# Optimization experiments

Hardware: AMD Instinct MI355X
Metric: run time of the kernel (lower is better)

The kernel has to match this reference:

```python
import jax, jax.numpy as jnp
import numpy as np

V, C, L, H, FF, T_MAX = 50257, 768, 12, 12, 3072, 1024
D = C // H  # head_dim = 64
B, T = 4, 1024


def setup_inputs() -> dict:
    key = jax.random.key(0)
    ks = jax.random.split(key, 20)
    s = 0.02
    inp = {
        'input_ids': jax.random.randint(ks[0], (B, T), 0, V),
        'tok_emb': jax.random.normal(ks[1], (V, C), jnp.float32) * s,
        'pos_emb': jax.random.normal(ks[2], (T_MAX, C), jnp.float32) * s,
        # per-layer stacked params; linear weights stored [in, out] (torch W.T)
        'qkv_w': jax.random.normal(ks[3], (L, C, 3 * C), jnp.float32) * s,
        'qkv_b': jnp.zeros((L, 3 * C), jnp.float32),
        'proj_w': jax.random.normal(ks[4], (L, C, C), jnp.float32) * (s / np.sqrt(2 * L)),
        'proj_b': jnp.zeros((L, C), jnp.float32),
        'ln1_w': jnp.ones((L, C), jnp.float32),
        'ln1_b': jnp.zeros((L, C), jnp.float32),
        'ln2_w': jnp.ones((L, C), jnp.float32),
        'ln2_b': jnp.zeros((L, C), jnp.float32),
        'fc1_w': jax.random.normal(ks[5], (L, C, FF), jnp.float32) * s,
        'fc1_b': jnp.zeros((L, FF), jnp.float32),
        'fc2_w': jax.random.normal(ks[6], (L, FF, C), jnp.float32) * s,
        'fc2_b': jnp.zeros((L, C), jnp.float32),
        'lnf_w': jnp.ones((C,), jnp.float32),
        'lnf_b': jnp.zeros((C,), jnp.float32),
    }
    return inp


def _ln(x, w, b, eps=1e-5):
    mu = jnp.mean(x, axis=-1, keepdims=True)
    var = jnp.var(x, axis=-1, keepdims=True)
    return (x - mu) * jax.lax.rsqrt(var + eps) * w + b


def _gpt_forward(input_ids, tok_emb, pos_emb, qkv_w, qkv_b, proj_w, proj_b,
                 ln1_w, ln1_b, ln2_w, ln2_b, fc1_w, fc1_b, fc2_w, fc2_b,
                 lnf_w, lnf_b):
    Bc, Tc = input_ids.shape
    x = tok_emb[input_ids] + pos_emb[:Tc][None, :, :]  # [B,T,C]
    causal = jnp.tril(jnp.ones((Tc, Tc), bool))  # [T,T]
    scale = 1.0 / np.sqrt(D)

    def block(x, p):
        (qw, qb, pw, pb, l1w, l1b, l2w, l2b, f1w, f1b, f2w, f2b) = p
        h = _ln(x, l1w, l1b)
        qkv = h @ qw + qb  # [B,T,3C]
        q, k, v = jnp.split(qkv, 3, axis=-1)
        q = q.reshape(Bc, Tc, H, D)
        k = k.reshape(Bc, Tc, H, D)
        v = v.reshape(Bc, Tc, H, D)
        att = jnp.einsum('bqhd,bkhd->bhqk', q, k) * scale
        att = jnp.where(causal[None, None], att, -jnp.inf)
        att = jax.nn.softmax(att, axis=-1)
        o = jnp.einsum('bhqk,bkhd->bqhd', att, v).reshape(Bc, Tc, C)
        x = x + o @ pw + pb
        h2 = _ln(x, l2w, l2b)
        m = jax.nn.gelu(h2 @ f1w + f1b, approximate=False) @ f2w + f2b
        return x + m, None

    params = (qkv_w, qkv_b, proj_w, proj_b, ln1_w, ln1_b, ln2_w, ln2_b,
              fc1_w, fc1_b, fc2_w, fc2_b)
    x, _ = jax.lax.scan(block, x, params)
    x = _ln(x, lnf_w, lnf_b)
    logits = x @ tok_emb.T  # tied lm_head, no bias
    return logits


def reference(input_ids, tok_emb, pos_emb, qkv_w, qkv_b, proj_w, proj_b,
              ln1_w, ln1_b, ln2_w, ln2_b, fc1_w, fc1_b, fc2_w, fc2_b,
              lnf_w, lnf_b):
    return _gpt_forward(input_ids, tok_emb, pos_emb, qkv_w, qkv_b, proj_w,
                        proj_b, ln1_w, ln1_b, ln2_w, ln2_b, fc1_w, fc1_b,
                        fc2_w, fc2_b, lnf_w, lnf_b)
```

## Files before the change

kernel.cpp:

```cpp
#include <hip/hip_runtime.h>
#include <hip/hip_bf16.h>


typedef __bf16 bh_t;
typedef __bf16 bfx4 __attribute__((ext_vector_type(4)));
typedef __bf16 bfx8 __attribute__((ext_vector_type(8)));
typedef float  fx4  __attribute__((ext_vector_type(4)));

#define CDIM 768
#define TSEQ 1024
#define NHEAD 12
#define HDIM 64
#define NLAYER 12
#define MROWS 4096
#define VOCAB 50257
#define VPAD  50432

__device__ __forceinline__ void gload_lds16(const void* g, void* l) {
  __builtin_amdgcn_global_load_lds(
      (const __attribute__((address_space(1))) void*)g,
      (__attribute__((address_space(3))) void*)l, 16, 0, 0);
}

__device__ __forceinline__ fx4 mfma16(bfx8 a, bfx8 b, fx4 c) {
  return __builtin_amdgcn_mfma_f32_16x16x32_bf16(a, b, c, 0, 0, 0);
}

__global__ __launch_bounds__(512, 4) void gemm256n(
    const bh_t* __restrict__ A, const bh_t* __restrict__ B,
    const float* __restrict__ bias, void* __restrict__ outp,
    int M, int N, int K, int lda, int flags)
{
  __shared__ bh_t A0[256][32], B0s[128][32];
  __shared__ bh_t A1[256][32], B1s[128][32];
  const int tid = threadIdx.x;
  const int wid = tid >> 6, lane = tid & 63;
  const int g = lane >> 4, r16 = lane & 15;
  const int wr = wid >> 1, wc = wid & 1;
  const int m0 = blockIdx.x * 256, n0 = blockIdx.y * 128;
  const int swk = (g ^ ((r16 >> 1) & 3)) * 8;

  const bh_t* Ab = A + (size_t)blockIdx.z * K + (size_t)m0 * lda;
  const bh_t* Bb = B + (size_t)blockIdx.z * K + (size_t)n0 * lda;
  const int nt = K >> 5;

  fx4 acc[4][4] = {};

  auto stage = [&](bh_t* dA, bh_t* dB, int t) {
    const int k0 = t << 5;
    #pragma unroll
    for (int j = 0; j < 2; ++j) {
      const int idx = j * 512 + tid;
      const int row = idx >> 2;
      const int slot = (idx & 3) ^ ((row >> 1) & 3);
      gload_lds16(Ab + (size_t)row * lda + k0 + slot * 8, dA + (size_t)idx * 8);
    }
    {
      const int idx = tid;
      const int row = idx >> 2;
      const int slot = (idx & 3) ^ ((row >> 1) & 3);
      gload_lds16(Bb + (size_t)row * lda + k0 + slot * 8, dB + (size_t)idx * 8);
    }
  };

#define N_TILE(CA, CB, NA, NB, T)                                             \
  {                                                                           \
    if ((T) + 1 < nt) stage(&NA[0][0], &NB[0][0], (T) + 1);                   \
    bfx8 av[4], bv[4];                                                        \
    _Pragma("unroll")                                                         \
    for (int ni = 0; ni < 4; ++ni)                                            \
      bv[ni] = *(const bfx8*)(&CB[wc * 64 + ni * 16 + r16][0] + swk);         \
    _Pragma("unroll")                                                         \
    for (int mi = 0; mi < 4; ++mi)                                            \
      av[mi] = *(const bfx8*)(&CA[wr * 64 + mi * 16 + r16][0] + swk);         \
    asm volatile("s_waitcnt lgkmcnt(0)" ::: "memory");                        \
    __builtin_amdgcn_s_setprio(1);                                            \
    _Pragma("unroll")                                                         \
    for (int mi = 0; mi < 4; ++mi)                                            \
      _Pragma("unroll")                                                       \
      for (int ni = 0; ni < 4; ++ni)                                          \
        acc[mi][ni] = mfma16(av[mi], bv[ni], acc[mi][ni]);                    \
    __builtin_amdgcn_s_setprio(0);                                            \
    asm volatile("s_waitcnt vmcnt(0)" ::: "memory");                          \
    __builtin_amdgcn_s_barrier();                                             \
    asm volatile("" ::: "memory");                                            \
  }

  stage(&A0[0][0], &B0s[0][0], 0);
  asm volatile("s_waitcnt vmcnt(0)" ::: "memory");
  __builtin_amdgcn_s_barrier();
  asm volatile("" ::: "memory");

  for (int t = 0; t < nt; t += 2) {
    N_TILE(A0, B0s, A1, B1s, t);
    N_TILE(A1, B1s, A0, B0s, t + 1);
  }
#undef N_TILE

  const bool hasBias = flags & 1, doGelu = flags & 4, outBf = flags & 8;
  float* outF = (float*)outp + (size_t)blockIdx.z * ((size_t)M * N);
  bh_t*  outB = (bh_t*)outp;
  #pragma unroll
  for (int mi = 0; mi < 4; ++mi) {
    const int rowb = m0 + wr * 64 + mi * 16 + 4 * g;
    #pragma unroll
    for (int ni = 0; ni < 4; ++ni) {
      const int col = n0 + wc * 64 + ni * 16 + r16;
      if (col >= N) continue;
      const float bv = hasBias ? bias[col] : 0.0f;
      #pragma unroll
      for (int rr = 0; rr < 4; ++rr) {
        const size_t idx = (size_t)(rowb + rr) * N + col;
        float v = acc[mi][ni][rr] + bv;
        if (doGelu) v = 0.5f * v * (1.0f + erff(v * 0.70710678118654752f));
        if (outBf) outB[idx] = (bh_t)v; else outF[idx] = v;
      }
    }
  }
}

__global__ __launch_bounds__(256) void skred_ln(
    const float* __restrict__ part, const float* __restrict__ bias,
    float* __restrict__ x, const float* __restrict__ w,
    const float* __restrict__ bb, bh_t* __restrict__ out, int S)
{
  const int wave = threadIdx.x >> 6, lane = threadIdx.x & 63;
  const int row = blockIdx.x * 4 + wave;
  const size_t base = (size_t)row * CDIM;
  const int off = lane * 4;
  const size_t stride = (size_t)MROWS * CDIM;

  float4 v0 = *(const float4*)(x + base + off);
  float4 v1 = *(const float4*)(x + base + 256 + off);
  float4 v2 = *(const float4*)(x + base + 512 + off);
  for (int s = 0; s < S; ++s) {
    const float* pr = part + s * stride + base;
    const float4 p0 = *(const float4*)(pr + off);
    const float4 p1 = *(const float4*)(pr + 256 + off);
    const float4 p2 = *(const float4*)(pr + 512 + off);
    v0.x += p0.x; v0.y += p0.y; v0.z += p0.z; v0.w += p0.w;
    v1.x += p1.x; v1.y += p1.y; v1.z += p1.z; v1.w += p1.w;
    v2.x += p2.x; v2.y += p2.y; v2.z += p2.z; v2.w += p2.w;
  }
  const float4 q0 = *(const float4*)(bias + off);
  const float4 q1 = *(const float4*)(bias + 256 + off);
  const float4 q2 = *(const float4*)(bias + 512 + off);
  v0.x += q0.x; v0.y += q0.y; v0.z += q0.z; v0.w += q0.w;
  v1.x += q1.x; v1.y += q1.y; v1.z += q1.z; v1.w += q1.w;
  v2.x += q2.x; v2.y += q2.y; v2.z += q2.z; v2.w += q2.w;
  *(float4*)(x + base + off) = v0;
  *(float4*)(x + base + 256 + off) = v1;
  *(float4*)(x + base + 512 + off) = v2;

  float s1 = v0.x + v0.y + v0.z + v0.w + v1.x + v1.y + v1.z + v1.w
           + v2.x + v2.y + v2.z + v2.w;
  float ss = v0.x*v0.x + v0.y*v0.y + v0.z*v0.z + v0.w*v0.w
           + v1.x*v1.x + v1.y*v1.y + v1.z*v1.z + v1.w*v1.w
           + v2.x*v2.x + v2.y*v2.y + v2.z*v2.z + v2.w*v2.w;
  #pragma unroll
  for (int d = 1; d < 64; d <<= 1) { s1 += __shfl_xor(s1, d); ss += __shfl_xor(ss, d); }
  const float mean = s1 * (1.0f / 768.0f);
  const float inv = rsqrtf(ss * (1.0f / 768.0f) - mean * mean + 1e-5f);
  bh_t* orow = out + base;

  const float4 w0 = *(const float4*)(w + off),       b0 = *(const float4*)(bb + off);
  const float4 w1 = *(const float4*)(w + 256 + off), b1 = *(const float4*)(bb + 256 + off);
  const float4 w2 = *(const float4*)(w + 512 + off), b2 = *(const float4*)(bb + 512 + off);
  bfx4 o;
  o[0] = (bh_t)((v0.x - mean) * inv * w0.x + b0.x);
  o[1] = (bh_t)((v0.y - mean) * inv * w0.y + b0.y);
  o[2] = (bh_t)((v0.z - mean) * inv * w0.z + b0.z);
  o[3] = (bh_t)((v0.w - mean) * inv * w0.w + b0.w);
  *(bfx4*)(orow + off) = o;
  o[0] = (bh_t)((v1.x - mean) * inv * w1.x + b1.x);
  o[1] = (bh_t)((v1.y - mean) * inv * w1.y + b1.y);
  o[2] = (bh_t)((v1.z - mean) * inv * w1.z + b1.z);
  o[3] = (bh_t)((v1.w - mean) * inv * w1.w + b1.w);
  *(bfx4*)(orow + 256 + off) = o;
  o[0] = (bh_t)((v2.x - mean) * inv * w2.x + b2.x);
  o[1] = (bh_t)((v2.y - mean) * inv * w2.y + b2.y);
  o[2] = (bh_t)((v2.z - mean) * inv * w2.z + b2.z);
  o[3] = (bh_t)((v2.w - mean) * inv * w2.w + b2.w);
  *(bfx4*)(orow + 512 + off) = o;
}

__global__ __launch_bounds__(256) void attn_fwd(
    const bh_t* __restrict__ qkv, const bh_t* __restrict__ vT,
    bh_t* __restrict__ outb)
{
  __shared__ bh_t P[4][16][56];
  const int wave = threadIdx.x >> 6, lane = threadIdx.x & 63;
  const int g = lane >> 4, r16 = lane & 15;
  const int gw = blockIdx.x * 4 + wave;
  const int qblk = gw & 63;
  const int bh = gw >> 6;
  const int h = bh % NHEAD, b = bh / NHEAD;
  const int qbase = qblk * 16;
  const int qidx = qbase + r16;

  const bh_t* qp = qkv + (size_t)(b * TSEQ + qbase + r16) * (3 * CDIM) + h * HDIM + 8 * g;
  const bfx8 qf0 = *(const bfx8*)qp;
  const bfx8 qf1 = *(const bfx8*)(qp + 32);

  fx4 o[4] = {};
  float m = -INFINITY, l = 0.0f;
  const int ntiles = qblk / 2 + 1;

  for (int t = 0; t < ntiles; ++t) {
    const int kv0 = t * 32;
    const bh_t* kp = qkv + (size_t)(b * TSEQ + kv0 + r16) * (3 * CDIM) + CDIM + h * HDIM + 8 * g;
    const bfx8 ka0 = *(const bfx8*)kp;
    const bfx8 ka1 = *(const bfx8*)(kp + 32);
    const bfx8 kb0 = *(const bfx8*)(kp + 16 * (3 * CDIM));
    const bfx8 kb1 = *(const bfx8*)(kp + 16 * (3 * CDIM) + 32);
    fx4 s0 = {}, s1 = {};
    s0 = mfma16(ka0, qf0, s0); s0 = mfma16(ka1, qf1, s0);
    s1 = mfma16(kb0, qf0, s1); s1 = mfma16(kb1, qf1, s1);

    float mx = -INFINITY;
    float sv0[4], sv1[4];
    #pragma unroll
    for (int rr = 0; rr < 4; ++rr) {
      const int kva = kv0 + 4 * g + rr;
      const int kvb = kva + 16;
      sv0[rr] = (kva <= qidx) ? s0[rr] * 0.125f : -INFINITY;
      sv1[rr] = (kvb <= qidx) ? s1[rr] * 0.125f : -INFINITY;
      mx = fmaxf(mx, fmaxf(sv0[rr], sv1[rr]));
    }
    mx = fmaxf(mx, __shfl_xor(mx, 16));
    mx = fmaxf(mx, __shfl_xor(mx, 32));
    const float mnew = fmaxf(m, mx);
    const float corr = __expf(m - mnew);

    float ps = 0.0f;
    float pv0[4], pv1[4];
    #pragma unroll
    for (int rr = 0; rr < 4; ++rr) {
      pv0[rr] = __expf(sv0[rr] - mnew);
      pv1[rr] = __expf(sv1[rr] - mnew);
      ps += pv0[rr] + pv1[rr];
    }
    ps += __shfl_xor(ps, 16);
    ps += __shfl_xor(ps, 32);
    l = l * corr + ps;
    m = mnew;

    #pragma unroll
    for (int rr = 0; rr < 4; ++rr) {
      const float cr = __shfl(corr, 4 * g + rr);
      o[0][rr] *= cr; o[1][rr] *= cr; o[2][rr] *= cr; o[3][rr] *= cr;
    }

    bfx4 w0, w1;
    #pragma unroll
    for (int rr = 0; rr < 4; ++rr) { w0[rr] = (bh_t)pv0[rr]; w1[rr] = (bh_t)pv1[rr]; }
    *(bfx4*)&P[wave][r16][4 * g]      = w0;
    *(bfx4*)&P[wave][r16][16 + 4 * g] = w1;
    __builtin_amdgcn_wave_barrier();
    const bfx8 pf = *(const bfx8*)&P[wave][r16][8 * g];

    #pragma unroll
    for (int fi = 0; fi < 4; ++fi) {
      const bh_t* vp = vT + (size_t)(bh * HDIM + fi * 16 + r16) * TSEQ + kv0 + 8 * g;
      const bfx8 vf = *(const bfx8*)vp;
      o[fi] = mfma16(pf, vf, o[fi]);
    }
  }

  #pragma unroll
  for (int rr = 0; rr < 4; ++rr) {
    const float lr = __shfl(l, 4 * g + rr);
    const float inv = 1.0f / lr;
    const int trow = b * TSEQ + qbase + 4 * g + rr;
    #pragma unroll
    for (int fi = 0; fi < 4; ++fi)
      outb[(size_t)trow * CDIM + h * HDIM + fi * 16 + r16] = (bh_t)(o[fi][rr] * inv);
  }
}

__global__ __launch_bounds__(256) void ln_fwd(
    const float* __restrict__ x, const float* __restrict__ w,
    const float* __restrict__ bb, bh_t* __restrict__ out)
{
  const int wave = threadIdx.x >> 6, lane = threadIdx.x & 63;
  const int row = blockIdx.x * 4 + wave;
  const float* xr = x + (size_t)row * CDIM;
  const int off = lane * 4;
  const float4 v0 = *(const float4*)(xr + off);
  const float4 v1 = *(const float4*)(xr + 256 + off);
  const float4 v2 = *(const float4*)(xr + 512 + off);
  float s  = v0.x + v0.y + v0.z + v0.w + v1.x + v1.y + v1.z + v1.w
           + v2.x + v2.y + v2.z + v2.w;
  float ss = v0.x*v0.x + v0.y*v0.y + v0.z*v0.z + v0.w*v0.w
           + v1.x*v1.x + v1.y*v1.y + v1.z*v1.z + v1.w*v1.w
           + v2.x*v2.x + v2.y*v2.y + v2.z*v2.z + v2.w*v2.w;
  #pragma unroll
  for (int d = 1; d < 64; d <<= 1) { s += __shfl_xor(s, d); ss += __shfl_xor(ss, d); }
  const float mean = s * (1.0f / 768.0f);
  const float inv = rsqrtf(ss * (1.0f / 768.0f) - mean * mean + 1e-5f);
  bh_t* orow = out + (size_t)row * CDIM;

  const float4 w0 = *(const float4*)(w + off),  b0 = *(const float4*)(bb + off);
  const float4 w1 = *(const float4*)(w + 256 + off), b1 = *(const float4*)(bb + 256 + off);
  const float4 w2 = *(const float4*)(w + 512 + off), b2 = *(const float4*)(bb + 512 + off);
  bfx4 o;
  o[0] = (bh_t)((v0.x - mean) * inv * w0.x + b0.x);
  o[1] = (bh_t)((v0.y - mean) * inv * w0.y + b0.y);
  o[2] = (bh_t)((v0.z - mean) * inv * w0.z + b0.z);
  o[3] = (bh_t)((v0.w - mean) * inv * w0.w + b0.w);
  *(bfx4*)(orow + off) = o;
  o[0] = (bh_t)((v1.x - mean) * inv * w1.x + b1.x);
  o[1] = (bh_t)((v1.y - mean) * inv * w1.y + b1.y);
  o[2] = (bh_t)((v1.z - mean) * inv * w1.z + b1.z);
  o[3] = (bh_t)((v1.w - mean) * inv * w1.w + b1.w);
  *(bfx4*)(orow + 256 + off) = o;
  o[0] = (bh_t)((v2.x - mean) * inv * w2.x + b2.x);
  o[1] = (bh_t)((v2.y - mean) * inv * w2.y + b2.y);
  o[2] = (bh_t)((v2.z - mean) * inv * w2.z + b2.z);
  o[3] = (bh_t)((v2.w - mean) * inv * w2.w + b2.w);
  *(bfx4*)(orow + 512 + off) = o;
}

__global__ void embed_k(const int* __restrict__ ids, const float* __restrict__ tok,
                        const float* __restrict__ pos, float* __restrict__ x)
{
  const int bt = blockIdx.x;
  const int t = bt & (TSEQ - 1);
  const int id = ids[bt];
  const float* tr = tok + (size_t)id * CDIM;
  const float* pr = pos + (size_t)t * CDIM;
  float* xr = x + (size_t)bt * CDIM;
  for (int j = threadIdx.x; j < CDIM; j += 256) xr[j] = tr[j] + pr[j];
}

__global__ void tconv(const float* __restrict__ in, bh_t* __restrict__ out, int R, int Cn)
{
  __shared__ float tile[32][33];
  const size_t msz = (size_t)R * Cn;
  in  += msz * blockIdx.z;
  out += msz * blockIdx.z;
  const int tx = threadIdx.x & 31, ty = threadIdx.x >> 5;
  const int c0 = blockIdx.x * 32, r0 = blockIdx.y * 32;
  #pragma unroll
  for (int i = 0; i < 32; i += 8)
    tile[ty + i][tx] = in[(size_t)(r0 + ty + i) * Cn + c0 + tx];
  __syncthreads();
  #pragma unroll
  for (int i = 0; i < 32; i += 8)
    out[(size_t)(c0 + ty + i) * R + r0 + tx] = (bh_t)tile[tx][ty + i];
}

__global__ void embconv(const float* __restrict__ in, bh_t* __restrict__ out)
{
  const size_t i4 = ((size_t)blockIdx.x * 256 + threadIdx.x) * 4;
  if (i4 >= (size_t)VPAD * CDIM) return;
  const size_t vlim = (size_t)VOCAB * CDIM;
  float4 f = make_float4(0.f, 0.f, 0.f, 0.f);
  if (i4 < vlim) f = *(const float4*)(in + i4);
  bfx4 o;
  o[0] = (bh_t)f.x; o[1] = (bh_t)f.y; o[2] = (bh_t)f.z; o[3] = (bh_t)f.w;
  *(bfx4*)(out + i4) = o;
}

__global__ void vtrans(const bh_t* __restrict__ qkv, bh_t* __restrict__ vT)
{
  __shared__ bh_t tile[32][34];
  const int bh = blockIdx.z;
  const int b = bh / NHEAD, h = bh % NHEAD;
  const int d0 = blockIdx.x * 32, t0 = blockIdx.y * 32;
  const int tx = threadIdx.x & 31, ty = threadIdx.x >> 5;
  #pragma unroll
  for (int i = 0; i < 32; i += 8)
    tile[ty + i][tx] = qkv[(size_t)(b * TSEQ + t0 + ty + i) * (3 * CDIM) + 2 * CDIM + h * HDIM + d0 + tx];
  __syncthreads();
  #pragma unroll
  for (int i = 0; i < 32; i += 8)
    vT[(size_t)(bh * HDIM + d0 + ty + i) * TSEQ + t0 + tx] = tile[tx][ty + i];
}

extern "C" void kernel_launch(void* const* d_in, const int* in_sizes, int n_in,
                              void* d_out, int out_size, void* d_ws, size_t ws_size,
                              hipStream_t stream)
{
  (void)in_sizes; (void)n_in; (void)out_size; (void)ws_size;
  const int*   ids    = (const int*)d_in[0];
  const float* tok    = (const float*)d_in[1];
  const float* pos    = (const float*)d_in[2];
  const float* qkv_w  = (const float*)d_in[3];
  const float* qkv_b  = (const float*)d_in[4];
  const float* proj_w = (const float*)d_in[5];
  const float* proj_b = (const float*)d_in[6];
  const float* ln1_w  = (const float*)d_in[7];
  const float* ln1_b  = (const float*)d_in[8];
  const float* ln2_w  = (const float*)d_in[9];
  const float* ln2_b  = (const float*)d_in[10];
  const float* fc1_w  = (const float*)d_in[11];
  const float* fc1_b  = (const float*)d_in[12];
  const float* fc2_w  = (const float*)d_in[13];
  const float* fc2_b  = (const float*)d_in[14];
  const float* lnf_w  = (const float*)d_in[15];
  const float* lnf_b  = (const float*)d_in[16];

  char* wp = (char*)d_ws;
  auto carve = [&](size_t bytes) { char* p = wp; wp += (bytes + 255) & ~(size_t)255; return p; };
  float* x     = (float*)carve((size_t)MROWS * CDIM * 4);
  bh_t*  hbuf  = (bh_t*)carve((size_t)MROWS * CDIM * 2);
  bh_t*  qkvb  = (bh_t*)carve((size_t)MROWS * 3 * CDIM * 2);
  bh_t*  vT    = (bh_t*)carve((size_t)48 * HDIM * TSEQ * 2);
  bh_t*  attno = (bh_t*)carve((size_t)MROWS * CDIM * 2);
  bh_t*  mlp1  = (bh_t*)carve((size_t)MROWS * 3072 * 2);
  bh_t*  embT  = (bh_t*)carve((size_t)VPAD * CDIM * 2);

  char* op = (char*)d_out;
  auto carveO = [&](size_t bytes) { char* p = op; op += (bytes + 255) & ~(size_t)255; return p; };
  bh_t* qkvwT  = (bh_t*)carveO((size_t)NLAYER * 3 * CDIM * CDIM * 2);
  bh_t* projwT = (bh_t*)carveO((size_t)NLAYER * CDIM * CDIM * 2);
  bh_t* fc1wT  = (bh_t*)carveO((size_t)NLAYER * 3072 * CDIM * 2);
  bh_t* fc2wT  = (bh_t*)carveO((size_t)NLAYER * CDIM * 3072 * 2);
  float* skpart = (float*)carveO((size_t)4 * MROWS * CDIM * 4);

  tconv<<<dim3(2304 / 32, 768 / 32, NLAYER), 256, 0, stream>>>(qkv_w, qkvwT, 768, 2304);
  tconv<<<dim3(768 / 32, 768 / 32, NLAYER), 256, 0, stream>>>(proj_w, projwT, 768, 768);
  tconv<<<dim3(3072 / 32, 768 / 32, NLAYER), 256, 0, stream>>>(fc1_w, fc1wT, 768, 3072);
  tconv<<<dim3(768 / 32, 3072 / 32, NLAYER), 256, 0, stream>>>(fc2_w, fc2wT, 3072, 768);
  embconv<<<((VPAD * CDIM / 4) + 255) / 256, 256, 0, stream>>>(tok, embT);
  embed_k<<<MROWS, 256, 0, stream>>>(ids, tok, pos, x);

  ln_fwd<<<MROWS / 4, 256, 0, stream>>>(x, ln1_w, ln1_b, hbuf);
  for (int l = 0; l < NLAYER; ++l) {
    gemm256n<<<dim3(16, 18), 512, 0, stream>>>(hbuf, qkvwT + (size_t)l * 3 * CDIM * CDIM,
        qkv_b + l * 3 * CDIM, qkvb, MROWS, 3 * CDIM, CDIM, CDIM, 1 | 8);
    vtrans<<<dim3(2, 32, 48), 256, 0, stream>>>(qkvb, vT);
    attn_fwd<<<768, 256, 0, stream>>>(qkvb, vT, attno);
    gemm256n<<<dim3(16, 6, 4), 512, 0, stream>>>(attno,
        projwT + (size_t)l * CDIM * CDIM, nullptr, skpart, MROWS, CDIM, 192, CDIM, 0);
    skred_ln<<<MROWS / 4, 256, 0, stream>>>(skpart, proj_b + l * CDIM, x,
        ln2_w + l * CDIM, ln2_b + l * CDIM, hbuf, 4);
    gemm256n<<<dim3(16, 24), 512, 0, stream>>>(hbuf, fc1wT + (size_t)l * 3072 * CDIM,
        fc1_b + l * 3072, mlp1, MROWS, 3072, CDIM, CDIM, 1 | 4 | 8);
    gemm256n<<<dim3(16, 6, 4), 512, 0, stream>>>(mlp1, fc2wT + (size_t)l * CDIM * 3072,
        nullptr, skpart, MROWS, CDIM, 768, 3072, 0);
    const float* nw = (l + 1 < NLAYER) ? ln1_w + (l + 1) * CDIM : lnf_w;
    const float* nb = (l + 1 < NLAYER) ? ln1_b + (l + 1) * CDIM : lnf_b;
    skred_ln<<<MROWS / 4, 256, 0, stream>>>(skpart, fc2_b + l * CDIM, x, nw, nb, hbuf, 4);
  }
  gemm256n<<<dim3(16, 393), 512, 0, stream>>>(hbuf, embT, nullptr,
      (float*)d_out, MROWS, VOCAB, CDIM, CDIM, 0);
}
```

Before: 3.696 ms.

## Replace block-shared GEMM tiles with per-wave private LDS tiles, removing barriers

The 256x128, 512-thread GEMM is replaced by a 128x128, 256-thread kernel. Each wave stages its own 64-row A and B slices into private double-buffered LDS and waits with a partial vmcnt, so the per-k-step block barrier is gone. The cost is less data reuse: waves in the same row or column of the block each load the same operand slices, roughly doubling global/L2 and LDS fill traffic per FLOP. The vocab padding for the tied embedding is also trimmed to exactly 393 tiles of 128, so the padded embedding copy is smaller.

```diff
diff --git a/kernel.cpp b/kernel.cpp
--- a/kernel.cpp
+++ b/kernel.cpp
@@ -14,7 +14,6 @@
 #define NLAYER 12
 #define MROWS 4096
 #define VOCAB 50257
-#define VPAD  50432
 
 __device__ __forceinline__ void gload_lds16(const void* g, void* l) {
   __builtin_amdgcn_global_load_lds(
@@ -26,53 +25,64 @@
   return __builtin_amdgcn_mfma_f32_16x16x32_bf16(a, b, c, 0, 0, 0);
 }
 
-__global__ __launch_bounds__(512, 4) void gemm256n(
+__global__ __launch_bounds__(256, 2) void gemm_wp(
     const bh_t* __restrict__ A, const bh_t* __restrict__ B,
     const float* __restrict__ bias, void* __restrict__ outp,
     int M, int N, int K, int lda, int flags)
 {
-  __shared__ bh_t A0[256][32], B0s[128][32];
-  __shared__ bh_t A1[256][32], B1s[128][32];
+  __shared__ bh_t LA[2][4][64][32];
+  __shared__ bh_t LB[2][4][64][32];
   const int tid = threadIdx.x;
   const int wid = tid >> 6, lane = tid & 63;
   const int g = lane >> 4, r16 = lane & 15;
   const int wr = wid >> 1, wc = wid & 1;
-  const int m0 = blockIdx.x * 256, n0 = blockIdx.y * 128;
+  const int m0 = blockIdx.x * 128, n0 = blockIdx.y * 128;
   const int swk = (g ^ ((r16 >> 1) & 3)) * 8;
 
-  const bh_t* Ab = A + (size_t)blockIdx.z * K + (size_t)m0 * lda;
-  const bh_t* Bb = B + (size_t)blockIdx.z * K + (size_t)n0 * lda;
+  const bh_t* AbW = A + (size_t)blockIdx.z * K + (size_t)(m0 + wr * 64) * lda;
+  const bh_t* BbW = B + (size_t)blockIdx.z * K + (size_t)(n0 + wc * 64) * lda;
   const int nt = K >> 5;
+
+  bh_t* myA0 = &LA[0][wid][0][0];
+  bh_t* myA1 = &LA[1][wid][0][0];
+  bh_t* myB0 = &LB[0][wid][0][0];
+  bh_t* myB1 = &LB[1][wid][0][0];
 
   fx4 acc[4][4] = {};
 
   auto stage = [&](bh_t* dA, bh_t* dB, int t) {
     const int k0 = t << 5;
     #pragma unroll
-    for (int j = 0; j < 2; ++j) {
-      const int idx = j * 512 + tid;
+    for (int j = 0; j < 4; ++j) {
+      const int idx = j * 64 + lane;
       const int row = idx >> 2;
       const int slot = (idx & 3) ^ ((row >> 1) & 3);
-      gload_lds16(Ab + (size_t)row * lda + k0 + slot * 8, dA + (size_t)idx * 8);
-    }
-    {
-      const int idx = tid;
+      gload_lds16(AbW + (size_t)row * lda + k0 + slot * 8, dA + (size_t)idx * 8);
+    }
+    #pragma unroll
+    for (int j = 0; j < 4; ++j) {
+      const int idx = j * 64 + lane;
       const int row = idx >> 2;
       const int slot = (idx & 3) ^ ((row >> 1) & 3);
-      gload_lds16(Bb + (size_t)row * lda + k0 + slot * 8, dB + (size_t)idx * 8);
+      gload_lds16(BbW + (size_t)row * lda + k0 + slot * 8, dB + (size_t)idx * 8);
     }
   };
 
-#define N_TILE(CA, CB, NA, NB, T)                                             \
+#define WP_TILE(CA, CB, NA, NB, T)                                            \
   {                                                                           \
-    if ((T) + 1 < nt) stage(&NA[0][0], &NB[0][0], (T) + 1);                   \
+    if ((T) + 1 < nt) {                                                       \
+      stage(NA, NB, (T) + 1);                                                 \
+      asm volatile("s_waitcnt vmcnt(8)" ::: "memory");                        \
+    } else {                                                                  \
+      asm volatile("s_waitcnt vmcnt(0)" ::: "memory");                        \
+    }                                                                         \
     bfx8 av[4], bv[4];                                                        \
     _Pragma("unroll")                                                         \
     for (int ni = 0; ni < 4; ++ni)                                            \
-      bv[ni] = *(const bfx8*)(&CB[wc * 64 + ni * 16 + r16][0] + swk);         \
+      bv[ni] = *(const bfx8*)(CB + (size_t)(ni * 16 + r16) * 32 + swk);       \
     _Pragma("unroll")                                                         \
     for (int mi = 0; mi < 4; ++mi)                                            \
-      av[mi] = *(const bfx8*)(&CA[wr * 64 + mi * 16 + r16][0] + swk);         \
+      av[mi] = *(const bfx8*)(CA + (size_t)(mi * 16 + r16) * 32 + swk);       \
     asm volatile("s_waitcnt lgkmcnt(0)" ::: "memory");                        \
     __builtin_amdgcn_s_setprio(1);                                            \
     _Pragma("unroll")                                                         \
@@ -81,21 +91,14 @@
       for (int ni = 0; ni < 4; ++ni)                                          \
         acc[mi][ni] = mfma16(av[mi], bv[ni], acc[mi][ni]);                    \
     __builtin_amdgcn_s_setprio(0);                                            \
-    asm volatile("s_waitcnt vmcnt(0)" ::: "memory");                          \
-    __builtin_amdgcn_s_barrier();                                             \
-    asm volatile("" ::: "memory");                                            \
-  }
-
-  stage(&A0[0][0], &B0s[0][0], 0);
-  asm volatile("s_waitcnt vmcnt(0)" ::: "memory");
-  __builtin_amdgcn_s_barrier();
-  asm volatile("" ::: "memory");
-
+  }
+
+  stage(myA0, myB0, 0);
   for (int t = 0; t < nt; t += 2) {
-    N_TILE(A0, B0s, A1, B1s, t);
-    N_TILE(A1, B1s, A0, B0s, t + 1);
-  }
-#undef N_TILE
+    WP_TILE(myA0, myB0, myA1, myB1, t);
+    WP_TILE(myA1, myB1, myA0, myB0, t + 1);
+  }
+#undef WP_TILE
 
   const bool hasBias = flags & 1, doGelu = flags & 4, outBf = flags & 8;
   float* outF = (float*)outp + (size_t)blockIdx.z * ((size_t)M * N);
@@ -350,6 +353,7 @@
     out[(size_t)(c0 + ty + i) * R + r0 + tx] = (bh_t)tile[tx][ty + i];
 }
 
+#define VPAD 50304
 __global__ void embconv(const float* __restrict__ in, bh_t* __restrict__ out)
 {
   const size_t i4 = ((size_t)blockIdx.x * 256 + threadIdx.x) * 4;
@@ -428,22 +432,22 @@
 
   ln_fwd<<<MROWS / 4, 256, 0, stream>>>(x, ln1_w, ln1_b, hbuf);
   for (int l = 0; l < NLAYER; ++l) {
-    gemm256n<<<dim3(16, 18), 512, 0, stream>>>(hbuf, qkvwT + (size_t)l * 3 * CDIM * CDIM,
+    gemm_wp<<<dim3(32, 18), 256, 0, stream>>>(hbuf, qkvwT + (size_t)l * 3 * CDIM * CDIM,
         qkv_b + l * 3 * CDIM, qkvb, MROWS, 3 * CDIM, CDIM, CDIM, 1 | 8);
     vtrans<<<dim3(2, 32, 48), 256, 0, stream>>>(qkvb, vT);
     attn_fwd<<<768, 256, 0, stream>>>(qkvb, vT, attno);
-    gemm256n<<<dim3(16, 6, 4), 512, 0, stream>>>(attno,
+    gemm_wp<<<dim3(32, 6, 4), 256, 0, stream>>>(attno,
         projwT + (size_t)l * CDIM * CDIM, nullptr, skpart, MROWS, CDIM, 192, CDIM, 0);
     skred_ln<<<MROWS / 4, 256, 0, stream>>>(skpart, proj_b + l * CDIM, x,
         ln2_w + l * CDIM, ln2_b + l * CDIM, hbuf, 4);
-    gemm256n<<<dim3(16, 24), 512, 0, stream>>>(hbuf, fc1wT + (size_t)l * 3072 * CDIM,
+    gemm_wp<<<dim3(32, 24), 256, 0, stream>>>(hbuf, fc1wT + (size_t)l * 3072 * CDIM,
         fc1_b + l * 3072, mlp1, MROWS, 3072, CDIM, CDIM, 1 | 4 | 8);
-    gemm256n<<<dim3(16, 6, 4), 512, 0, stream>>>(mlp1, fc2wT + (size_t)l * CDIM * 3072,
+    gemm_wp<<<dim3(32, 6, 4), 256, 0, stream>>>(mlp1, fc2wT + (size_t)l * CDIM * 3072,
         nullptr, skpart, MROWS, CDIM, 768, 3072, 0);
     const float* nw = (l + 1 < NLAYER) ? ln1_w + (l + 1) * CDIM : lnf_w;
     const float* nb = (l + 1 < NLAYER) ? ln1_b + (l + 1) * CDIM : lnf_b;
     skred_ln<<<MROWS / 4, 256, 0, stream>>>(skpart, fc2_b + l * CDIM, x, nw, nb, hbuf, 4);
   }
-  gemm256n<<<dim3(16, 393), 512, 0, stream>>>(hbuf, embT, nullptr,
+  gemm_wp<<<dim3(32, 393), 256, 0, stream>>>(hbuf, embT, nullptr,
       (float*)d_out, MROWS, VOCAB, CDIM, CDIM, 0);
 }
```

Measured after the change: 4.543 ms. +22.9%, slower.

## Replace split-K proj/fc2 GEMMs with 128x64-tile GEMM fusing bias and residual

Applied to the files above, without the earlier changes.

The N=768 projection and fc2 GEMMs used to run as split-K over 4 slices, writing fp32 partials that a separate kernel reduced before LayerNorm. A new 128x64-tile GEMM now covers the full K and adds bias plus the residual straight into x, so the partial buffer and its reduction traffic go away and plain LayerNorm follows. Each block now walks the full K (up to 3072) and the grid is 384 blocks of 256 threads. VPAD also shrinks, which reduces the padded embedding conversion work.

```diff
diff --git a/kernel.cpp b/kernel.cpp
--- a/kernel.cpp
+++ b/kernel.cpp
@@ -14,7 +14,7 @@
 #define NLAYER 12
 #define MROWS 4096
 #define VOCAB 50257
-#define VPAD  50432
+#define VPAD  50304
 
 __device__ __forceinline__ void gload_lds16(const void* g, void* l) {
   __builtin_amdgcn_global_load_lds(
@@ -119,162 +119,96 @@
   }
 }
 
-__global__ __launch_bounds__(256) void skred_ln(
-    const float* __restrict__ part, const float* __restrict__ bias,
-    float* __restrict__ x, const float* __restrict__ w,
-    const float* __restrict__ bb, bh_t* __restrict__ out, int S)
-{
-  const int wave = threadIdx.x >> 6, lane = threadIdx.x & 63;
-  const int row = blockIdx.x * 4 + wave;
-  const size_t base = (size_t)row * CDIM;
-  const int off = lane * 4;
-  const size_t stride = (size_t)MROWS * CDIM;
-
-  float4 v0 = *(const float4*)(x + base + off);
-  float4 v1 = *(const float4*)(x + base + 256 + off);
-  float4 v2 = *(const float4*)(x + base + 512 + off);
-  for (int s = 0; s < S; ++s) {
-    const float* pr = part + s * stride + base;
-    const float4 p0 = *(const float4*)(pr + off);
-    const float4 p1 = *(const float4*)(pr + 256 + off);
-    const float4 p2 = *(const float4*)(pr + 512 + off);
-    v0.x += p0.x; v0.y += p0.y; v0.z += p0.z; v0.w += p0.w;
-    v1.x += p1.x; v1.y += p1.y; v1.z += p1.z; v1.w += p1.w;
-    v2.x += p2.x; v2.y += p2.y; v2.z += p2.z; v2.w += p2.w;
-  }
-  const float4 q0 = *(const float4*)(bias + off);
-  const float4 q1 = *(const float4*)(bias + 256 + off);
-  const float4 q2 = *(const float4*)(bias + 512 + off);
-  v0.x += q0.x; v0.y += q0.y; v0.z += q0.z; v0.w += q0.w;
-  v1.x += q1.x; v1.y += q1.y; v1.z += q1.z; v1.w += q1.w;
-  v2.x += q2.x; v2.y += q2.y; v2.z += q2.z; v2.w += q2.w;
-  *(float4*)(x + base + off) = v0;
-  *(float4*)(x + base + 256 + off) = v1;
-  *(float4*)(x + base + 512 + off) = v2;
-
-  float s1 = v0.x + v0.y + v0.z + v0.w + v1.x + v1.y + v1.z + v1.w
-           + v2.x + v2.y + v2.z + v2.w;
-  float ss = v0.x*v0.x + v0.y*v0.y + v0.z*v0.z + v0.w*v0.w
-           + v1.x*v1.x + v1.y*v1.y + v1.z*v1.z + v1.w*v1.w
-           + v2.x*v2.x + v2.y*v2.y + v2.z*v2.z + v2.w*v2.w;
-  #pragma unroll
-  for (int d = 1; d < 64; d <<= 1) { s1 += __shfl_xor(s1, d); ss += __shfl_xor(ss, d); }
-  const float mean = s1 * (1.0f / 768.0f);
-  const float inv = rsqrtf(ss * (1.0f / 768.0f) - mean * mean + 1e-5f);
-  bh_t* orow = out + base;
-
-  const float4 w0 = *(const float4*)(w + off),       b0 = *(const float4*)(bb + off);
-  const float4 w1 = *(const float4*)(w + 256 + off), b1 = *(const float4*)(bb + 256 + off);
-  const float4 w2 = *(const float4*)(w + 512 + off), b2 = *(const float4*)(bb + 512 + off);
-  bfx4 o;
-  o[0] = (bh_t)((v0.x - mean) * inv * w0.x + b0.x);
-  o[1] = (bh_t)((v0.y - mean) * inv * w0.y + b0.y);
-  o[2] = (bh_t)((v0.z - mean) * inv * w0.z + b0.z);
-  o[3] = (bh_t)((v0.w - mean) * inv * w0.w + b0.w);
-  *(bfx4*)(orow + off) = o;
-  o[0] = (bh_t)((v1.x - mean) * inv * w1.x + b1.x);
-  o[1] = (bh_t)((v1.y - mean) * inv * w1.y + b1.y);
-  o[2] = (bh_t)((v1.z - mean) * inv * w1.z + b1.z);
-  o[3] = (bh_t)((v1.w - mean) * inv * w1.w + b1.w);
-  *(bfx4*)(orow + 256 + off) = o;
-  o[0] = (bh_t)((v2.x - mean) * inv * w2.x + b2.x);
-  o[1] = (bh_t)((v2.y - mean) * inv * w2.y + b2.y);
-  o[2] = (bh_t)((v2.z - mean) * inv * w2.z + b2.z);
-  o[3] = (bh_t)((v2.w - mean) * inv * w2.w + b2.w);
-  *(bfx4*)(orow + 512 + off) = o;
-}
-
-__global__ __launch_bounds__(256) void attn_fwd(
-    const bh_t* __restrict__ qkv, const bh_t* __restrict__ vT,
-    bh_t* __restrict__ outb)
-{
-  __shared__ bh_t P[4][16][56];
-  const int wave = threadIdx.x >> 6, lane = threadIdx.x & 63;
+__global__ __launch_bounds__(256, 4) void gemm_n64(
+    const bh_t* __restrict__ A, const bh_t* __restrict__ B,
+    const float* __restrict__ bias, const float* __restrict__ resid,
+    void* __restrict__ outp, int M, int N, int K, int lda, int flags)
+{
+  __shared__ bh_t A0[128][32], B0s[64][32];
+  __shared__ bh_t A1[128][32], B1s[64][32];
+  const int tid = threadIdx.x;
+  const int wid = tid >> 6, lane = tid & 63;
   const int g = lane >> 4, r16 = lane & 15;
-  const int gw = blockIdx.x * 4 + wave;
-  const int qblk = gw & 63;
-  const int bh = gw >> 6;
-  const int h = bh % NHEAD, b = bh / NHEAD;
-  const int qbase = qblk * 16;
-  const int qidx = qbase + r16;
-
-  const bh_t* qp = qkv + (size_t)(b * TSEQ + qbase + r16) * (3 * CDIM) + h * HDIM + 8 * g;
-  const bfx8 qf0 = *(const bfx8*)qp;
-  const bfx8 qf1 = *(const bfx8*)(qp + 32);
-
-  fx4 o[4] = {};
-  float m = -INFINITY, l = 0.0f;
-  const int ntiles = qblk / 2 + 1;
-
-  for (int t = 0; t < ntiles; ++t) {
-    const int kv0 = t * 32;
-    const bh_t* kp = qkv + (size_t)(b * TSEQ + kv0 + r16) * (3 * CDIM) + CDIM + h * HDIM + 8 * g;
-    const bfx8 ka0 = *(const bfx8*)kp;
-    const bfx8 ka1 = *(const bfx8*)(kp + 32);
-    const bfx8 kb0 = *(const bfx8*)(kp + 16 * (3 * CDIM));
-    const bfx8 kb1 = *(const bfx8*)(kp + 16 * (3 * CDIM) + 32);
-    fx4 s0 = {}, s1 = {};
-    s0 = mfma16(ka0, qf0, s0); s0 = mfma16(ka1, qf1, s0);
-    s1 = mfma16(kb0, qf0, s1); s1 = mfma16(kb1, qf1, s1);
-
-    float mx = -INFINITY;
-    float sv0[4], sv1[4];
-    #pragma unroll
-    for (int rr = 0; rr < 4; ++rr) {
-      const int kva = kv0 + 4 * g + rr;
-      const int kvb = kva + 16;
-      sv0[rr] = (kva <= qidx) ? s0[rr] * 0.125f : -INFINITY;
-      sv1[rr] = (kvb <= qidx) ? s1[rr] * 0.125f : -INFINITY;
-      mx = fmaxf(mx, fmaxf(sv0[rr], sv1[rr]));
-    }
-    mx = fmaxf(mx, __shfl_xor(mx, 16));
-    mx = fmaxf(mx, __shfl_xor(mx, 32));
-    const float mnew = fmaxf(m, mx);
-    const float corr = __expf(m - mnew);
-
-    float ps = 0.0f;
-    float pv0[4], pv1[4];
-    #pragma unroll
-    for (int rr = 0; rr < 4; ++rr) {
-      pv0[rr] = __expf(sv0[rr] - mnew);
-      pv1[rr] = __expf(sv1[rr] - mnew);
-      ps += pv0[rr] + pv1[rr];
-    }
-    ps += __shfl_xor(ps, 16);
-    ps += __shfl_xor(ps, 32);
-    l = l * corr + ps;
-    m = mnew;
-
-    #pragma unroll
-    for (int rr = 0; rr < 4; ++rr) {
-      const float cr = __shfl(corr, 4 * g + rr);
-      o[0][rr] *= cr; o[1][rr] *= cr; o[2][rr] *= cr; o[3][rr] *= cr;
-    }
-
-    bfx4 w0, w1;
-    #pragma unroll
-    for (int rr = 0; rr < 4; ++rr) { w0[rr] = (bh_t)pv0[rr]; w1[rr] = (bh_t)pv1[rr]; }
-    *(bfx4*)&P[wave][r16][4 * g]      = w0;
-    *(bfx4*)&P[wave][r16][16 + 4 * g] = w1;
-    __builtin_amdgcn_wave_barrier();
-    const bfx8 pf = *(const bfx8*)&P[wave][r16][8 * g];
-
-    #pragma unroll
-    for (int fi = 0; fi < 4; ++fi) {
-      const bh_t* vp = vT + (size_t)(bh * HDIM + fi * 16 + r16) * TSEQ + kv0 + 8 * g;
-      const bfx8 vf = *(const bfx8*)vp;
-      o[fi] = mfma16(pf, vf, o[fi]);
-    }
-  }
-
-  #pragma unroll
-  for (int rr = 0; rr < 4; ++rr) {
-    const float lr = __shfl(l, 4 * g + rr);
-    const float inv = 1.0f / lr;
-    const int trow = b * TSEQ + qbase + 4 * g + rr;
-    #pragma unroll
-    for (int fi = 0; fi < 4; ++fi)
-      outb[(size_t)trow * CDIM + h * HDIM + fi * 16 + r16] = (bh_t)(o[fi][rr] * inv);
+  const int wr = wid >> 1, wc = wid & 1;
+  const int m0 = blockIdx.x * 128, n0 = blockIdx.y * 64;
+  const int swk = (g ^ ((r16 >> 1) & 3)) * 8;
+
+  const bh_t* Ab = A + (size_t)m0 * lda;
+  const bh_t* Bb = B + (size_t)n0 * lda;
+  const int nt = K >> 5;
+
+  fx4 acc[4][2] = {};
+
+  auto stage = [&](bh_t* dA, bh_t* dB, int t) {
+    const int k0 = t << 5;
+    #pragma unroll
+    for (int j = 0; j < 2; ++j) {
+      const int idx = j * 256 + tid;
+      const int row = idx >> 2;
+      const int slot = (idx & 3) ^ ((row >> 1) & 3);
+      gload_lds16(Ab + (size_t)row * lda + k0 + slot * 8, dA + (size_t)idx * 8);
+    }
+    {
+      const int idx = tid;
+      const int row = idx >> 2;
+      const int slot = (idx & 3) ^ ((row >> 1) & 3);
+      gload_lds16(Bb + (size_t)row * lda + k0 + slot * 8, dB + (size_t)idx * 8);
+    }
+  };
+
+#define N64_TILE(CA, CB, NA, NB, T)                                           \
+  {                                                                           \
+    if ((T) + 1 < nt) stage(&NA[0][0], &NB[0][0], (T) + 1);                   \
+    bfx8 av[4], bv[2];                                                        \
+    _Pragma("unroll")                                                         \
+    for (int ni = 0; ni < 2; ++ni)                                            \
+      bv[ni] = *(const bfx8*)(&CB[wc * 32 + ni * 16 + r16][0] + swk);         \
+    _Pragma("unroll")                                                         \
+    for (int mi = 0; mi < 4; ++mi)                                            \
+      av[mi] = *(const bfx8*)(&CA[wr * 64 + mi * 16 + r16][0] + swk);         \
+    asm volatile("s_waitcnt lgkmcnt(0)" ::: "memory");                        \
+    __builtin_amdgcn_s_setprio(1);                                            \
+    _Pragma("unroll")                                                         \
+    for (int mi = 0; mi < 4; ++mi)                                            \
+      _Pragma("unroll")                                                       \
+      for (int ni = 0; ni < 2; ++ni)                                          \
+        acc[mi][ni] = mfma16(av[mi], bv[ni], acc[mi][ni]);                    \
+    __builtin_amdgcn_s_setprio(0);                                            \
+    asm volatile("s_waitcnt vmcnt(0)" ::: "memory");                          \
+    __builtin_amdgcn_s_barrier();                                             \
+    asm volatile("" ::: "memory");                                            \
+  }
+
+  stage(&A0[0][0], &B0s[0][0], 0);
+  asm volatile("s_waitcnt vmcnt(0)" ::: "memory");
+  __builtin_amdgcn_s_barrier();
+  asm volatile("" ::: "memory");
+
+  for (int t = 0; t < nt; t += 2) {
+    N64_TILE(A0, B0s, A1, B1s, t);
+    N64_TILE(A1, B1s, A0, B0s, t + 1);
+  }
+#undef N64_TILE
+
+  const bool hasBias = flags & 1, hasRes = flags & 2, outBf = flags & 8;
+  float* outF = (float*)outp;
+  bh_t*  outB = (bh_t*)outp;
+  #pragma unroll
+  for (int mi = 0; mi < 4; ++mi) {
+    const int rowb = m0 + wr * 64 + mi * 16 + 4 * g;
+    #pragma unroll
+    for (int ni = 0; ni < 2; ++ni) {
+      const int col = n0 + wc * 32 + ni * 16 + r16;
+      if (col >= N) continue;
+      const float bv = hasBias ? bias[col] : 0.0f;
+      #pragma unroll
+      for (int rr = 0; rr < 4; ++rr) {
+        const size_t idx = (size_t)(rowb + rr) * N + col;
+        float v = acc[mi][ni][rr] + bv;
+        if (hasRes) v += resid[idx];
+        if (outBf) outB[idx] = (bh_t)v; else outF[idx] = v;
+      }
+    }
   }
 }
 
@@ -321,6 +255,100 @@
   *(bfx4*)(orow + 512 + off) = o;
 }
 
+__global__ __launch_bounds__(256) void attn_fwd(
+    const bh_t* __restrict__ qkv, const bh_t* __restrict__ vT,
+    bh_t* __restrict__ outb)
+{
+  __shared__ bh_t P[4][16][56];
+  const int wave = threadIdx.x >> 6, lane = threadIdx.x & 63;
+  const int g = lane >> 4, r16 = lane & 15;
+  const int gw = blockIdx.x * 4 + wave;
+  const int qblk = gw & 63;
+  const int bh = gw >> 6;
+  const int h = bh % NHEAD, b = bh / NHEAD;
+  const int qbase = qblk * 16;
+  const int qidx = qbase + r16;
+
+  const bh_t* qp = qkv + (size_t)(b * TSEQ + qbase + r16) * (3 * CDIM) + h * HDIM + 8 * g;
+  const bfx8 qf0 = *(const bfx8*)qp;
+  const bfx8 qf1 = *(const bfx8*)(qp + 32);
+
+  fx4 o[4] = {};
+  float m = -INFINITY, l = 0.0f;
+  const int ntiles = qblk / 2 + 1;
+
+  for (int t = 0; t < ntiles; ++t) {
+    const int kv0 = t * 32;
+    const bh_t* kp = qkv + (size_t)(b * TSEQ + kv0 + r16) * (3 * CDIM) + CDIM + h * HDIM + 8 * g;
+    const bfx8 ka0 = *(const bfx8*)kp;
+    const bfx8 ka1 = *(const bfx8*)(kp + 32);
+    const bfx8 kb0 = *(const bfx8*)(kp + 16 * (3 * CDIM));
+    const bfx8 kb1 = *(const bfx8*)(kp + 16 * (3 * CDIM) + 32);
+    fx4 s0 = {}, s1 = {};
+    s0 = mfma16(ka0, qf0, s0); s0 = mfma16(ka1, qf1, s0);
+    s1 = mfma16(kb0, qf0, s1); s1 = mfma16(kb1, qf1, s1);
+
+    float mx = -INFINITY;
+    float sv0[4], sv1[4];
+    #pragma unroll
+    for (int rr = 0; rr < 4; ++rr) {
+      const int kva = kv0 + 4 * g + rr;
+      const int kvb = kva + 16;
+      sv0[rr] = (kva <= qidx) ? s0[rr] * 0.125f : -INFINITY;
+      sv1[rr] = (kvb <= qidx) ? s1[rr] * 0.125f : -INFINITY;
+      mx = fmaxf(mx, fmaxf(sv0[rr], sv1[rr]));
+    }
+    mx = fmaxf(mx, __shfl_xor(mx, 16));
+    mx = fmaxf(mx, __shfl_xor(mx, 32));
+    const float mnew = fmaxf(m, mx);
+    const float corr = __expf(m - mnew);
+
+    float ps = 0.0f;
+    float pv0[4], pv1[4];
+    #pragma unroll
+    for (int rr = 0; rr < 4; ++rr) {
+      pv0[rr] = __expf(sv0[rr] - mnew);
+      pv1[rr] = __expf(sv1[rr] - mnew);
+      ps += pv0[rr] + pv1[rr];
+    }
+    ps += __shfl_xor(ps, 16);
+    ps += __shfl_xor(ps, 32);
+    l = l * corr + ps;
+    m = mnew;
+
+    #pragma unroll
+    for (int rr = 0; rr < 4; ++rr) {
+      const float cr = __shfl(corr, 4 * g + rr);
+      o[0][rr] *= cr; o[1][rr] *= cr; o[2][rr] *= cr; o[3][rr] *= cr;
+    }
+
+    bfx4 w0, w1;
+    #pragma unroll
+    for (int rr = 0; rr < 4; ++rr) { w0[rr] = (bh_t)pv0[rr]; w1[rr] = (bh_t)pv1[rr]; }
+    *(bfx4*)&P[wave][r16][4 * g]      = w0;
+    *(bfx4*)&P[wave][r16][16 + 4 * g] = w1;
+    __builtin_amdgcn_wave_barrier();
+    const bfx8 pf = *(const bfx8*)&P[wave][r16][8 * g];
+
+    #pragma unroll
+    for (int fi = 0; fi < 4; ++fi) {
+      const bh_t* vp = vT + (size_t)(bh * HDIM + fi * 16 + r16) * TSEQ + kv0 + 8 * g;
+      const bfx8 vf = *(const bfx8*)vp;
+      o[fi] = mfma16(pf, vf, o[fi]);
+    }
+  }
+
+  #pragma unroll
+  for (int rr = 0; rr < 4; ++rr) {
+    const float lr = __shfl(l, 4 * g + rr);
+    const float inv = 1.0f / lr;
+    const int trow = b * TSEQ + qbase + 4 * g + rr;
+    #pragma unroll
+    for (int fi = 0; fi < 4; ++fi)
+      outb[(size_t)trow * CDIM + h * HDIM + fi * 16 + r16] = (bh_t)(o[fi][rr] * inv);
+  }
+}
+
 __global__ void embed_k(const int* __restrict__ ids, const float* __restrict__ tok,
                         const float* __restrict__ pos, float* __restrict__ x)
 {
@@ -417,7 +445,6 @@
   bh_t* projwT = (bh_t*)carveO((size_t)NLAYER * CDIM * CDIM * 2);
   bh_t* fc1wT  = (bh_t*)carveO((size_t)NLAYER * 3072 * CDIM * 2);
   bh_t* fc2wT  = (bh_t*)carveO((size_t)NLAYER * CDIM * 3072 * 2);
-  float* skpart = (float*)carveO((size_t)4 * MROWS * CDIM * 4);
 
   tconv<<<dim3(2304 / 32, 768 / 32, NLAYER), 256, 0, stream>>>(qkv_w, qkvwT, 768, 2304);
   tconv<<<dim3(768 / 32, 768 / 32, NLAYER), 256, 0, stream>>>(proj_w, projwT, 768, 768);
@@ -432,17 +459,18 @@
         qkv_b + l * 3 * CDIM, qkvb, MROWS, 3 * CDIM, CDIM, CDIM, 1 | 8);
     vtrans<<<dim3(2, 32, 48), 256, 0, stream>>>(qkvb, vT);
     attn_fwd<<<768, 256, 0, stream>>>(qkvb, vT, attno);
-    gemm256n<<<dim3(16, 6, 4), 512, 0, stream>>>(attno,
-        projwT + (size_t)l * CDIM * CDIM, nullptr, skpart, MROWS, CDIM, 192, CDIM, 0);
-    skred_ln<<<MROWS / 4, 256, 0, stream>>>(skpart, proj_b + l * CDIM, x,
-        ln2_w + l * CDIM, ln2_b + l * CDIM, hbuf, 4);
+    gemm_n64<<<dim3(32, 12), 256, 0, stream>>>(attno,
+        projwT + (size_t)l * CDIM * CDIM, proj_b + l * CDIM, x, x,
+        MROWS, CDIM, CDIM, CDIM, 1 | 2);
+    ln_fwd<<<MROWS / 4, 256, 0, stream>>>(x, ln2_w + l * CDIM, ln2_b + l * CDIM, hbuf);
     gemm256n<<<dim3(16, 24), 512, 0, stream>>>(hbuf, fc1wT + (size_t)l * 3072 * CDIM,
         fc1_b + l * 3072, mlp1, MROWS, 3072, CDIM, CDIM, 1 | 4 | 8);
-    gemm256n<<<dim3(16, 6, 4), 512, 0, stream>>>(mlp1, fc2wT + (size_t)l * CDIM * 3072,
-        nullptr, skpart, MROWS, CDIM, 768, 3072, 0);
+    gemm_n64<<<dim3(32, 12), 256, 0, stream>>>(mlp1,
+        fc2wT + (size_t)l * CDIM * 3072, fc2_b + l * CDIM, x, x,
+        MROWS, CDIM, 3072, 3072, 1 | 2);
     const float* nw = (l + 1 < NLAYER) ? ln1_w + (l + 1) * CDIM : lnf_w;
     const float* nb = (l + 1 < NLAYER) ? ln1_b + (l + 1) * CDIM : lnf_b;
-    skred_ln<<<MROWS / 4, 256, 0, stream>>>(skpart, fc2_b + l * CDIM, x, nw, nb, hbuf, 4);
+    ln_fwd<<<MROWS / 4, 256, 0, stream>>>(x, nw, nb, hbuf);
   }
   gemm256n<<<dim3(16, 393), 512, 0, stream>>>(hbuf, embT, nullptr,
       (float*)d_out, MROWS, VOCAB, CDIM, CDIM, 0);
```

New measurement: 3.925 ms. 6.2% more time.
